# Kernel optimization log

Measured on AMD Instinct MI355X. Metric: run time of the kernel, lower is better.

## Reference

```python
import jax, jax.numpy as jnp
import numpy as np

KERNEL_MUL = 2.0
KERNEL_NUM = 5


def setup_inputs() -> dict:
    key = jax.random.key(0)
    k1, k2 = jax.random.split(key)
    N, D = 4096, 256
    source = jax.random.normal(k1, (N, D), dtype=jnp.float32)
    target = jax.random.normal(k2, (N, D), dtype=jnp.float32)
    return {"source": source, "target": target}


def reference(source, target):
    ns = source.shape[0]
    total = jnp.concatenate([source, target], axis=0)  # [2N, D]
    n = total.shape[0]
    # Pairwise squared L2 distance via GEMM trick (same math as expand+sub+square+sum)
    sq = jnp.sum(total * total, axis=1)               # [2N]
    gram = total @ total.T                             # [2N, 2N]
    l2 = sq[:, None] + sq[None, :] - 2.0 * gram        # [2N, 2N]
    # Bandwidth from detached distances (torch uses .data)
    l2_sg = jax.lax.stop_gradient(l2)
    bandwidth = jnp.sum(l2_sg) / (n * n - n)
    bandwidth = bandwidth / (KERNEL_MUL ** (KERNEL_NUM // 2))
    bws = bandwidth * (KERNEL_MUL ** jnp.arange(KERNEL_NUM, dtype=l2.dtype))  # [K]
    # Multi-kernel Gaussian RBF sum: sum_k exp(-l2 / bw_k)
    kernels = jnp.exp(-l2[None, :, :] / bws[:, None, None]).sum(axis=0)  # [2N, 2N]
    XX = kernels[:ns, :ns]
    YY = kernels[ns:, ns:]
    XY = kernels[:ns, ns:]
    YX = kernels[ns:, :ns]
    loss = jnp.mean(XX) + jnp.mean(YY) - jnp.mean(XY) - jnp.mean(YX)
    return loss
```

## Files before the change

### kernel.cpp

```cpp
#include <hip/hip_runtime.h>
#include <hip/hip_bf16.h>
#include <stdint.h>


#define NROW 8192
#define NS   4096
#define DD   256
#define TILE 128
#define BK2  32
#define NTB  64
#define NBLK (NTB*(NTB+1)/2)
#define K1B  128

typedef __bf16 bf16_t;
typedef __bf16 bf16x8 __attribute__((ext_vector_type(8)));
typedef __bf16 bf16x4 __attribute__((ext_vector_type(4)));
typedef float  f32x4  __attribute__((ext_vector_type(4)));

#define OFF_CPAR 0
#define OFF_SQ   1024
#define OFF_CS   (OFF_SQ + 8192*4)
#define OFF_SS   (OFF_CS + K1B*256*4)
#define OFF_PART (OFF_SS + 1024)
#define OFF_TBF  (1<<18)

__device__ __forceinline__ void async16(const void* g, void* l) {
  __builtin_amdgcn_global_load_lds(
      (const __attribute__((address_space(1))) void*)(uintptr_t)g,
      (__attribute__((address_space(3))) void*)(uintptr_t)l, 16, 0, 0);
}

__global__ __launch_bounds__(256) void k1_prep(const float* __restrict__ src,
                                               const float* __restrict__ tgt,
                                               float* __restrict__ sq,
                                               float* __restrict__ cs_part,
                                               float* __restrict__ ss_part,
                                               bf16_t* __restrict__ tbf) {
  const int b = blockIdx.x, tid = threadIdx.x;
  const int w = tid >> 6, lane = tid & 63;
  float4 csum = make_float4(0.f, 0.f, 0.f, 0.f);
  float wss = 0.f;
  for (int r = 0; r < 16; ++r) {
    const int row = b * 64 + w * 16 + r;
    const float* rp = (row < NS) ? (src + (size_t)row * DD)
                                 : (tgt + (size_t)(row - NS) * DD);
    float4 v = ((const float4*)rp)[lane];
    bf16x4 o;
    o[0] = (bf16_t)v.x; o[1] = (bf16_t)v.y; o[2] = (bf16_t)v.z; o[3] = (bf16_t)v.w;
    *(bf16x4*)(tbf + (size_t)row * DD + lane * 4) = o;
    float s2 = v.x*v.x + v.y*v.y + v.z*v.z + v.w*v.w;
    #pragma unroll
    for (int off = 32; off >= 1; off >>= 1) s2 += __shfl_xor(s2, off);
    if (lane == 0) { sq[row] = s2; wss += s2; }
    csum.x += v.x; csum.y += v.y; csum.z += v.z; csum.w += v.w;
  }
  __shared__ float cls[4][256];
  __shared__ float sls[4];
  ((float4*)cls[w])[lane] = csum;
  if (lane == 0) sls[w] = wss;
  __syncthreads();
  cs_part[b * 256 + tid] = cls[0][tid] + cls[1][tid] + cls[2][tid] + cls[3][tid];
  if (tid == 0) ss_part[b] = sls[0] + sls[1] + sls[2] + sls[3];
}

__global__ __launch_bounds__(256) void k2_bw(const float* __restrict__ cs_part,
                                             const float* __restrict__ ss_part,
                                             float* __restrict__ cpar) {
  const int tid = threadIdx.x, w = tid >> 6, lane = tid & 63;
  float c = 0.f;
  for (int b = 0; b < K1B; ++b) c += cs_part[b * 256 + tid];
  double csq = (double)c * (double)c;
  double ssq = (tid < K1B) ? (double)ss_part[tid] : 0.0;
  #pragma unroll
  for (int off = 32; off >= 1; off >>= 1) {
    csq += __shfl_xor(csq, off);
    ssq += __shfl_xor(ssq, off);
  }
  __shared__ double rc[4], rs[4];
  if (lane == 0) { rc[w] = csq; rs[w] = ssq; }
  __syncthreads();
  if (tid == 0) {
    double C = rc[0] + rc[1] + rc[2] + rc[3];
    double S = rs[0] + rs[1] + rs[2] + rs[3];
    const double n = (double)NROW;
    double suml2 = 2.0 * n * S - 2.0 * C;
    double bw0 = suml2 / (n * n - n) / 4.0;
    cpar[0] = (float)(1.4426950408889634 / (16.0 * bw0));
  }
}


__device__ __forceinline__ void stage(const bf16_t* __restrict__ Ag,
                                      const bf16_t* __restrict__ Bg,
                                      bf16_t* As, bf16_t* Bs,
                                      int kt, int tid, int wbase) {
  #pragma unroll
  for (int it = 0; it < 2; ++it) {
    const int c  = it * 256 + tid;
    const int r  = c >> 2;
    const int sc = (c & 3) ^ ((r >> 1) & 3);
    const bf16_t* gsrcA = Ag + (size_t)r * DD + kt * BK2 + sc * 8;
    const bf16_t* gsrcB = Bg + (size_t)r * DD + kt * BK2 + sc * 8;
    char* da = (char*)As + (size_t)(it * 256 + wbase) * 16;
    char* db = (char*)Bs + (size_t)(it * 256 + wbase) * 16;
    async16(gsrcA, da);
    async16(gsrcB, db);
  }
}

__global__ __launch_bounds__(256) void k3_mmd(const bf16_t* __restrict__ tbf,
                                              const float* __restrict__ sqg,
                                              const float* __restrict__ cpar,
                                              float* __restrict__ part) {
  __shared__ __align__(16) bf16_t As[2][TILE * BK2];
  __shared__ __align__(16) bf16_t Bs[2][TILE * BK2];
  __shared__ float red[4];

  const int t = blockIdx.x;
  int bi = (int)((sqrtf(8.0f * (float)t + 1.0f) - 1.0f) * 0.5f);
  while ((bi + 1) * (bi + 2) / 2 <= t) ++bi;
  while (bi * (bi + 1) / 2 > t) --bi;
  const int bj = t - bi * (bi + 1) / 2;

  const int tid = threadIdx.x;
  const int w = tid >> 6, lane = tid & 63;
  const int m0 = (w >> 1) * 64, n0 = (w & 1) * 64;
  const int wbase = tid & ~63;

  const float cE = cpar[0];

  f32x4 acc[4][4] = {};

  const bf16_t* Ag = tbf + (size_t)bi * TILE * DD;
  const bf16_t* Bg = tbf + (size_t)bj * TILE * DD;

  const int kidx = (((lane >> 4) ^ ((lane >> 1) & 3)) * 8);
  const int lrow = lane & 15;

  stage(Ag, Bg, As[0], Bs[0], 0, tid, wbase);
  asm volatile("s_waitcnt vmcnt(0)" ::: "memory");
  __builtin_amdgcn_s_barrier();
  __builtin_amdgcn_sched_barrier(0);

  #pragma unroll
  for (int kt = 0; kt < 8; ++kt) {
    const int cur = kt & 1;
    if (kt < 7)
      stage(Ag, Bg, As[cur ^ 1], Bs[cur ^ 1], kt + 1, tid, wbase);

    bf16x8 af[4], bfr[4];
    #pragma unroll
    for (int mi = 0; mi < 4; ++mi)
      af[mi] = *(const bf16x8*)(As[cur] + (m0 + mi * 16 + lrow) * BK2 + kidx);
    #pragma unroll
    for (int ni = 0; ni < 4; ++ni)
      bfr[ni] = *(const bf16x8*)(Bs[cur] + (n0 + ni * 16 + lrow) * BK2 + kidx);
    #pragma unroll
    for (int mi = 0; mi < 4; ++mi)
      #pragma unroll
      for (int ni = 0; ni < 4; ++ni)
        acc[mi][ni] = __builtin_amdgcn_mfma_f32_16x16x32_bf16(
            af[mi], bfr[ni], acc[mi][ni], 0, 0, 0);

    if (kt < 7) {
      asm volatile("s_waitcnt vmcnt(0)" ::: "memory");
      __builtin_amdgcn_s_barrier();
      __builtin_amdgcn_sched_barrier(0);
    }
  }

  const float c2 = 2.0f * cE;
  float bjv[4];
  #pragma unroll
  for (int ni = 0; ni < 4; ++ni)
    bjv[ni] = sqg[bj * TILE + n0 + ni * 16 + lrow] * cE;

  float tsum = 0.f;
  #pragma unroll
  for (int mi = 0; mi < 4; ++mi) {
    float ai[4];
    #pragma unroll
    for (int r = 0; r < 4; ++r)
      ai[r] = sqg[bi * TILE + m0 + mi * 16 + (lane >> 4) * 4 + r] * cE;
    #pragma unroll
    for (int ni = 0; ni < 4; ++ni) {
      #pragma unroll
      for (int r = 0; r < 4; ++r) {
        const float g = acc[mi][ni][r];
        const float e = fmaf(g, c2, -(ai[r] + bjv[ni]));
        const float v   = __builtin_amdgcn_exp2f(e);
        const float v2  = v * v;
        const float v4  = v2 * v2;
        const float v8  = v4 * v4;
        const float v16 = v8 * v8;
        tsum += v + v2 + v4 + v8 + v16;
      }
    }
  }
  #pragma unroll
  for (int off = 32; off >= 1; off >>= 1) tsum += __shfl_xor(tsum, off);
  if (lane == 0) red[w] = tsum;
  __syncthreads();
  if (tid == 0) {
    const float s    = red[0] + red[1] + red[2] + red[3];
    const float sign = ((bi < NS / TILE) == (bj < NS / TILE)) ? 1.f : -1.f;
    const float wt   = (bi == bj) ? 1.f : 2.f;
    part[t] = s * sign * wt;
  }
}

__global__ __launch_bounds__(256) void k4_fin(const float* __restrict__ part,
                                              float* __restrict__ out) {
  const int tid = threadIdx.x, w = tid >> 6, lane = tid & 63;
  double s = 0.0;
  for (int i = tid; i < NBLK; i += 256) s += (double)part[i];
  #pragma unroll
  for (int off = 32; off >= 1; off >>= 1) s += __shfl_xor(s, off);
  __shared__ double rd[4];
  if (lane == 0) rd[w] = s;
  __syncthreads();
  if (tid == 0)
    out[0] = (float)((rd[0] + rd[1] + rd[2] + rd[3]) /
                     ((double)NS * (double)NS));
}

extern "C" void kernel_launch(void* const* d_in, const int* in_sizes, int n_in,
                              void* d_out, int out_size, void* d_ws, size_t ws_size,
                              hipStream_t stream) {
  const float* src = (const float*)d_in[0];
  const float* tgt = (const float*)d_in[1];
  char* ws = (char*)d_ws;
  float*  cpar = (float*)(ws + OFF_CPAR);
  float*  sq   = (float*)(ws + OFF_SQ);
  float*  csp  = (float*)(ws + OFF_CS);
  float*  ssp  = (float*)(ws + OFF_SS);
  float*  part = (float*)(ws + OFF_PART);
  bf16_t* tbf  = (bf16_t*)(ws + OFF_TBF);

  k1_prep<<<K1B, 256, 0, stream>>>(src, tgt, sq, csp, ssp, tbf);
  k2_bw  <<<1,   256, 0, stream>>>(csp, ssp, cpar);
  k3_mmd <<<NBLK,256, 0, stream>>>(tbf, sq, cpar, part);
  k4_fin <<<1,   256, 0, stream>>>(part, (float*)d_out);
}
```

Measured before the change: 109.4 us.

## Give each wave private LDS staging to remove block-wide barriers in GEMM loop

Each of the four waves now stages its own 64-row A and B sub-tiles into a private LDS region instead of sharing one block-wide tile. This removes all s_barrier calls from the k-loop, and a partial vmcnt wait lets the next stage's loads stay in flight while the current one is computed. The cost is that rows shared between waves are loaded twice, doubling global/L2 traffic per block and LDS usage (64KB vs 32KB), which may reduce occupancy.

```diff
diff --git a/kernel.cpp b/kernel.cpp
--- a/kernel.cpp
+++ b/kernel.cpp
@@ -90,30 +90,11 @@
 }
 
 
-__device__ __forceinline__ void stage(const bf16_t* __restrict__ Ag,
-                                      const bf16_t* __restrict__ Bg,
-                                      bf16_t* As, bf16_t* Bs,
-                                      int kt, int tid, int wbase) {
-  #pragma unroll
-  for (int it = 0; it < 2; ++it) {
-    const int c  = it * 256 + tid;
-    const int r  = c >> 2;
-    const int sc = (c & 3) ^ ((r >> 1) & 3);
-    const bf16_t* gsrcA = Ag + (size_t)r * DD + kt * BK2 + sc * 8;
-    const bf16_t* gsrcB = Bg + (size_t)r * DD + kt * BK2 + sc * 8;
-    char* da = (char*)As + (size_t)(it * 256 + wbase) * 16;
-    char* db = (char*)Bs + (size_t)(it * 256 + wbase) * 16;
-    async16(gsrcA, da);
-    async16(gsrcB, db);
-  }
-}
-
 __global__ __launch_bounds__(256) void k3_mmd(const bf16_t* __restrict__ tbf,
                                               const float* __restrict__ sqg,
                                               const float* __restrict__ cpar,
                                               float* __restrict__ part) {
-  __shared__ __align__(16) bf16_t As[2][TILE * BK2];
-  __shared__ __align__(16) bf16_t Bs[2][TILE * BK2];
+  __shared__ __align__(16) bf16_t WS[4][2][2][64 * BK2];
   __shared__ float red[4];
 
   const int t = blockIdx.x;
@@ -125,7 +106,6 @@
   const int tid = threadIdx.x;
   const int w = tid >> 6, lane = tid & 63;
   const int m0 = (w >> 1) * 64, n0 = (w & 1) * 64;
-  const int wbase = tid & ~63;
 
   const float cE = cpar[0];
 
@@ -134,39 +114,51 @@
   const bf16_t* Ag = tbf + (size_t)bi * TILE * DD;
   const bf16_t* Bg = tbf + (size_t)bj * TILE * DD;
 
+  const int srow = lane >> 2;
+  const int sc   = (lane & 3) ^ ((lane >> 3) & 3);
+  char* const wsbase = (char*)&WS[w][0][0][0];
+
   const int kidx = (((lane >> 4) ^ ((lane >> 1) & 3)) * 8);
   const int lrow = lane & 15;
 
-  stage(Ag, Bg, As[0], Bs[0], 0, tid, wbase);
-  asm volatile("s_waitcnt vmcnt(0)" ::: "memory");
-  __builtin_amdgcn_s_barrier();
-  __builtin_amdgcn_sched_barrier(0);
+  auto wstage = [&](int buf, int kt) {
+    #pragma unroll
+    for (int it = 0; it < 4; ++it) {
+      const int r = it * 16 + srow;
+      async16(Ag + (size_t)(m0 + r) * DD + kt * BK2 + sc * 8,
+              wsbase + buf * 8192 + it * 1024);
+      async16(Bg + (size_t)(n0 + r) * DD + kt * BK2 + sc * 8,
+              wsbase + buf * 8192 + 4096 + it * 1024);
+    }
+  };
+
+  wstage(0, 0);
 
   #pragma unroll
   for (int kt = 0; kt < 8; ++kt) {
-    const int cur = kt & 1;
-    if (kt < 7)
-      stage(Ag, Bg, As[cur ^ 1], Bs[cur ^ 1], kt + 1, tid, wbase);
-
+    if (kt < 7) {
+      wstage((kt + 1) & 1, kt + 1);
+      asm volatile("s_waitcnt vmcnt(8)" ::: "memory");
+    } else {
+      asm volatile("s_waitcnt vmcnt(0)" ::: "memory");
+    }
+    __builtin_amdgcn_sched_barrier(0);
+
+    const bf16_t* Aw = &WS[w][kt & 1][0][0];
+    const bf16_t* Bw = &WS[w][kt & 1][1][0];
     bf16x8 af[4], bfr[4];
     #pragma unroll
     for (int mi = 0; mi < 4; ++mi)
-      af[mi] = *(const bf16x8*)(As[cur] + (m0 + mi * 16 + lrow) * BK2 + kidx);
+      af[mi] = *(const bf16x8*)(Aw + (mi * 16 + lrow) * BK2 + kidx);
     #pragma unroll
     for (int ni = 0; ni < 4; ++ni)
-      bfr[ni] = *(const bf16x8*)(Bs[cur] + (n0 + ni * 16 + lrow) * BK2 + kidx);
+      bfr[ni] = *(const bf16x8*)(Bw + (ni * 16 + lrow) * BK2 + kidx);
     #pragma unroll
     for (int mi = 0; mi < 4; ++mi)
       #pragma unroll
       for (int ni = 0; ni < 4; ++ni)
         acc[mi][ni] = __builtin_amdgcn_mfma_f32_16x16x32_bf16(
             af[mi], bfr[ni], acc[mi][ni], 0, 0, 0);
-
-    if (kt < 7) {
-      asm volatile("s_waitcnt vmcnt(0)" ::: "memory");
-      __builtin_amdgcn_s_barrier();
-      __builtin_amdgcn_sched_barrier(0);
-    }
   }
 
   const float c2 = 2.0f * cE;
```

After: 109.8 us. About the same (+0.4%).
